# Kernel tuning notes

Measured on AMD Instinct MI355X. Metric: run time of the kernel, lower is better.

Reference implementation:

```python
import jax, jax.numpy as jnp
import numpy as np

B, H_IN, W_IN = 8192, 26, 26

def _conv(x, w, b):
    # NCHW conv, stride 1, padding 1 (as in OffConv2d: padding hardcoded to 1)
    y = jax.lax.conv_general_dilated(x, w, (1, 1), [(1, 1), (1, 1)],
                                     dimension_numbers=('NCHW', 'OIHW', 'NCHW'))
    return y + b[None, :, None, None]

def _grid_sample_bilinear_zeros(img, gx, gy):
    # img: (N,H,W), gx/gy: (N,H,W) normalized coords; matches torch grid_sample
    # mode='bilinear', padding_mode='zeros', align_corners=False
    N, H, W = img.shape
    ix = ((gx + 1.0) * W - 1.0) * 0.5
    iy = ((gy + 1.0) * H - 1.0) * 0.5
    x0 = jnp.floor(ix); y0 = jnp.floor(iy)
    x1 = x0 + 1.0;      y1 = y0 + 1.0
    wx1 = ix - x0; wx0 = 1.0 - wx1
    wy1 = iy - y0; wy0 = 1.0 - wy1
    bi = jnp.arange(N)[:, None, None]
    def gather(yy, xx):
        valid = (xx >= 0) & (xx < W) & (yy >= 0) & (yy < H)
        v = img[bi,
                jnp.clip(yy, 0, H - 1).astype(jnp.int32),
                jnp.clip(xx, 0, W - 1).astype(jnp.int32)]
        return jnp.where(valid, v, 0.0)
    return (gather(y0, x0) * wy0 * wx0 + gather(y0, x1) * wy0 * wx1 +
            gather(y1, x0) * wy1 * wx0 + gather(y1, x1) * wy1 * wx1)

def _off_conv(x, ws, bs, wx, bx, wy, by):
    s  = _conv(x, ws, bs)   # score  (B,C,H,W)
    gx = _conv(x, wx, bx)   # offset_x -> grid x coord
    gy = _conv(x, wy, by)   # offset_y -> grid y coord
    b, c, h, w = s.shape
    out = _grid_sample_bilinear_zeros(s.reshape(b * c, h, w),
                                      gx.reshape(b * c, h, w),
                                      gy.reshape(b * c, h, w))
    return out.reshape(b, c, h, w)

def _maxpool2(x):
    return jax.lax.reduce_window(x, -jnp.inf, jax.lax.max,
                                 (1, 1, 2, 2), (1, 1, 2, 2), 'VALID')

def setup_inputs() -> dict:
    key = jax.random.key(0)
    ks = jax.random.split(key, 20)
    r = lambda k, shp, s: (jax.random.normal(k, shp, dtype=jnp.float32) * s)
    inp = {
        'x':   r(ks[0], (B, H_IN, W_IN), 1.0),
        'w1s': r(ks[1], (6, 1, 5, 5), 0.2),  'b1s': r(ks[2], (6,), 0.1),
        'w1x': r(ks[3], (6, 1, 5, 5), 0.2),  'b1x': r(ks[4], (6,), 0.1),
        'w1y': r(ks[5], (6, 1, 5, 5), 0.2),  'b1y': r(ks[6], (6,), 0.1),
        'w2s': r(ks[7], (16, 6, 5, 5), 0.1), 'b2s': r(ks[8], (16,), 0.1),
        'w2x': r(ks[9], (16, 6, 5, 5), 0.1), 'b2x': r(ks[10], (16,), 0.1),
        'w2y': r(ks[11], (16, 6, 5, 5), 0.1),'b2y': r(ks[12], (16,), 0.1),
        'wf1': r(ks[13], (120, 400), 0.05),  'bf1': r(ks[14], (120,), 0.05),
        'wf2': r(ks[15], (84, 120), 0.05),   'bf2': r(ks[16], (84,), 0.05),
        'wf3': r(ks[17], (10, 84), 0.05),    'bf3': r(ks[18], (10,), 0.05),
    }
    return inp

def reference(x, w1s, b1s, w1x, b1x, w1y, b1y,
              w2s, b2s, w2x, b2x, w2y, b2y,
              wf1, bf1, wf2, bf2, wf3, bf3):
    h = x[:, None, :, :]                                   # (B,1,26,26)
    h = _maxpool2(jax.nn.relu(_off_conv(h, w1s, b1s, w1x, b1x, w1y, b1y)))  # (B,6,12,12)
    h = _maxpool2(jax.nn.relu(_off_conv(h, w2s, b2s, w2x, b2x, w2y, b2y)))  # (B,16,5,5)
    h = h.reshape(-1, 16 * 5 * 5)
    h = jax.nn.relu(h @ wf1.T + bf1)
    h = jax.nn.relu(h @ wf2.T + bf2)
    h = h @ wf3.T + bf3
    return jax.nn.softmax(h, axis=1)
```

## Files before the change

### kernel.cpp

```cpp
#include <hip/hip_runtime.h>
#include <math.h>

#define TPB 256
#define TPBA 448
#define TPBC 512

#define XS_S   34
#define SM1_S  26
#define SM1_C  624
#define H1P_R  18
#define H1P_C  252
#define H1P_I  1512

typedef float v2f __attribute__((ext_vector_type(2)));

__device__ __forceinline__ void pk_lo(v2f& acc, v2f ap, v2f w) {
    asm("v_pk_fma_f32 %0, %1, %2, %0 op_sel:[0,0,0] op_sel_hi:[0,1,1]"
        : "+v"(acc) : "v"(ap), "v"(w));
}
__device__ __forceinline__ void pk_hi(v2f& acc, v2f ap, v2f w) {
    asm("v_pk_fma_f32 %0, %1, %2, %0 op_sel:[1,0,0] op_sel_hi:[1,1,1]"
        : "+v"(acc) : "v"(ap), "v"(w));
}

#define OFF_WA_SX 0
#define OFF_WA_YY 300
#define OFF_WB_SX 464
#define OFF_WB_YY 5264
#define OFF_WF1T  7664
#define OFF_WF2T  55664
#define OFF_WF3T  65744
#define OFF_H1    66592
#define OFF_H2    7144480
#define WS_FLOATS 10421280ull
#define REQ_WS_BYTES (WS_FLOATS * 4ull)

__device__ __forceinline__ float bilin_zero_s(const float* __restrict__ img, int N, int S,
                                              float gx, float gy) {
    float fx = (gx + 1.0f) * (0.5f * (float)N) - 0.5f;
    float fy = (gy + 1.0f) * (0.5f * (float)N) - 0.5f;
    float x0 = floorf(fx), y0 = floorf(fy);
    float wx1 = fx - x0, wy1 = fy - y0;
    float wx0 = 1.0f - wx1, wy0 = 1.0f - wy1;
    float x1 = x0 + 1.0f, y1 = y0 + 1.0f;
    float Nm1 = (float)(N - 1);
    int xi0 = (int)fminf(fmaxf(x0, 0.0f), Nm1);
    int yi0 = (int)fminf(fmaxf(y0, 0.0f), Nm1);
    int xi1 = (int)fminf(fmaxf(x1, 0.0f), Nm1);
    int yi1 = (int)fminf(fmaxf(y1, 0.0f), Nm1);
    bool vx0 = (x0 >= 0.0f) && (x0 < (float)N);
    bool vx1 = (x1 >= 0.0f) && (x1 < (float)N);
    bool vy0 = (y0 >= 0.0f) && (y0 < (float)N);
    bool vy1 = (y1 >= 0.0f) && (y1 < (float)N);
    float v00 = (vy0 && vx0) ? img[yi0 * S + xi0] : 0.0f;
    float v01 = (vy0 && vx1) ? img[yi0 * S + xi1] : 0.0f;
    float v10 = (vy1 && vx0) ? img[yi1 * S + xi0] : 0.0f;
    float v11 = (vy1 && vx1) ? img[yi1 * S + xi1] : 0.0f;
    return v00 * wy0 * wx0 + v01 * wy0 * wx1 + v10 * wy1 * wx0 + v11 * wy1 * wx1;
}

__global__ __launch_bounds__(TPB) void lenet_prep(
    const float* __restrict__ w1s, const float* __restrict__ w1x, const float* __restrict__ w1y,
    const float* __restrict__ w2s, const float* __restrict__ w2x, const float* __restrict__ w2y,
    const float* __restrict__ wf1, const float* __restrict__ wf2, const float* __restrict__ wf3,
    float* __restrict__ wsf)
{
    int g = blockIdx.x * TPB + threadIdx.x;
    int stride = gridDim.x * TPB;
    for (int i = g; i < 75; i += stride) {
        int cp = i / 25, t = i % 25;
        int cA = (2 * cp) * 25 + t, cB = (2 * cp + 1) * 25 + t;
        float* p = wsf + OFF_WA_SX + i * 4;
        p[0] = w1s[cA]; p[1] = w1x[cA]; p[2] = w1s[cB]; p[3] = w1x[cB];
        wsf[OFF_WA_YY + i * 2 + 0] = w1y[cA];
        wsf[OFF_WA_YY + i * 2 + 1] = w1y[cB];
    }
    for (int e = g; e < 1200; e += stride) {
        int cp = e / 150, rem = e % 150;
        int iA = cp * 150 + rem, iB = (cp + 8) * 150 + rem;
        float* pp = wsf + OFF_WB_SX + e * 4;
        pp[0] = w2s[iA]; pp[1] = w2s[iB]; pp[2] = w2x[iA]; pp[3] = w2x[iB];
        wsf[OFF_WB_YY + e * 2 + 0] = w2y[iA];
        wsf[OFF_WB_YY + e * 2 + 1] = w2y[iB];
    }
    for (int i = g; i < 48000; i += stride) { int k = i / 120, o = i % 120; wsf[OFF_WF1T + i] = wf1[o * 400 + k]; }
    for (int i = g; i < 10080; i += stride) { int k = i / 84,  o = i % 84;  wsf[OFF_WF2T + i] = wf2[o * 120 + k]; }
    for (int i = g; i < 840;   i += stride) { int k = i / 10,  o = i % 10;  wsf[OFF_WF3T + i] = wf3[o * 84 + k]; }
}

__global__ __launch_bounds__(TPBA) void lenetA(
    const float* __restrict__ x, const float* __restrict__ wsf,
    const float* __restrict__ b1s, const float* __restrict__ b1x, const float* __restrict__ b1y,
    float* __restrict__ h1)
{
    __shared__ __align__(16) float xs_p[28 * XS_S];
    __shared__ float4 w1i[150];
    __shared__ float4 b1w[3];
    __shared__ v2f    b1yw[3];
    __shared__ __align__(16) float smap1[6 * SM1_C];

    const int tid = threadIdx.x, b = blockIdx.x;
    const float* xp = x + b * 676;
    for (int i = tid; i < 28 * XS_S; i += TPBA) {
        int r = i / XS_S, c = i % XS_S;
        float v = 0.0f;
        if (c < 28 && r >= 1 && r <= 26 && c >= 1 && c <= 26) v = xp[(r - 1) * 26 + (c - 1)];
        xs_p[i] = v;
    }
    if (tid < 150) w1i[tid] = ((const float4*)(wsf + OFF_WA_SX))[tid];
    if (tid < 3) {
        b1w[tid]  = make_float4(b1s[2 * tid], b1x[2 * tid], b1s[2 * tid + 1], b1x[2 * tid + 1]);
        b1yw[tid] = (v2f){b1y[2 * tid], b1y[2 * tid + 1]};
    }
    __syncthreads();

    const v2f* wyy = (const v2f*)(wsf + OFF_WA_YY);

    const int cp = tid / 144, p = tid % 144;
    const int py = p / 12, px = p % 12;
    const bool act = (tid < 432);

    float gxa[2][2][2], gya[2][2][2];
    if (act) {
        v2f aw[6][3];
        #pragma unroll
        for (int r = 0; r < 6; ++r) {
            const v2f* rp = (const v2f*)&xs_p[(2 * py + r) * XS_S + 2 * px];
            aw[r][0] = rp[0]; aw[r][1] = rp[1]; aw[r][2] = rp[2];
        }
        int c0 = 2 * cp, c1 = 2 * cp + 1;
        v2f a0[2][2], a1[2][2], ay[2][2];
        {
            float4 bb = b1w[cp];
            v2f i0 = {bb.x, bb.y};
            v2f i1 = {bb.z, bb.w};
            v2f iy = b1yw[cp];
            #pragma unroll
            for (int dy = 0; dy < 2; ++dy)
                #pragma unroll
                for (int dx = 0; dx < 2; ++dx) { a0[dy][dx] = i0; a1[dy][dx] = i1; ay[dy][dx] = iy; }
        }
        const float4* wp  = &w1i[cp * 25];
        const v2f*    wyp = wyy + cp * 25;
        #pragma unroll
        for (int ky = 0; ky < 5; ++ky)
            #pragma unroll
            for (int kx = 0; kx < 5; ++kx) {
                float4 w4 = wp[ky * 5 + kx];
                v2f wA = {w4.x, w4.y};
                v2f wB = {w4.z, w4.w};
                v2f wy = wyp[ky * 5 + kx];
                #pragma unroll
                for (int dy = 0; dy < 2; ++dy)
                    #pragma unroll
                    for (int dx = 0; dx < 2; ++dx) {
                        int cc = kx + dx;
                        v2f ap = aw[ky + dy][cc >> 1];
                        if ((cc & 1) == 0) {
                            pk_lo(a0[dy][dx], ap, wA);
                            pk_lo(a1[dy][dx], ap, wB);
                            pk_lo(ay[dy][dx], ap, wy);
                        } else {
                            pk_hi(a0[dy][dx], ap, wA);
                            pk_hi(a1[dy][dx], ap, wB);
                            pk_hi(ay[dy][dx], ap, wy);
                        }
                    }
            }
        {
            int base0 = (2 * py) * SM1_S + 2 * px;
            int base1 = base0 + SM1_S;
            *(v2f*)&smap1[c0 * SM1_C + base0] = (v2f){a0[0][0].x, a0[0][1].x};
            *(v2f*)&smap1[c0 * SM1_C + base1] = (v2f){a0[1][0].x, a0[1][1].x};
            *(v2f*)&smap1[c1 * SM1_C + base0] = (v2f){a1[0][0].x, a1[0][1].x};
            *(v2f*)&smap1[c1 * SM1_C + base1] = (v2f){a1[1][0].x, a1[1][1].x};
        }
        #pragma unroll
        for (int dy = 0; dy < 2; ++dy)
            #pragma unroll
            for (int dx = 0; dx < 2; ++dx) {
                gxa[0][dy][dx] = a0[dy][dx].y;  gya[0][dy][dx] = ay[dy][dx].x;
                gxa[1][dy][dx] = a1[dy][dx].y;  gya[1][dy][dx] = ay[dy][dx].y;
            }
    }
    __syncthreads();

    if (act) {
        #pragma unroll
        for (int ch = 0; ch < 2; ++ch) {
            int c = 2 * cp + ch;
            const float* smc = &smap1[c * SM1_C];
            float mx = 0.0f;
            #pragma unroll
            for (int dy = 0; dy < 2; ++dy)
                #pragma unroll
                for (int dx = 0; dx < 2; ++dx)
                    mx = fmaxf(mx, bilin_zero_s(smc, 24, SM1_S, gxa[ch][dy][dx], gya[ch][dy][dx]));
            h1[(size_t)b * 864 + c * 144 + p] = mx;
        }
    }
}

__global__ __launch_bounds__(TPB, 6) void lenetB(
    const float* __restrict__ h1, const float* __restrict__ wsf,
    const float* __restrict__ b2s, const float* __restrict__ b2x, const float* __restrict__ b2y,
    float* __restrict__ h2)
{
    __shared__ __align__(16) float h1p[2 * H1P_I];
    __shared__ __align__(16) float wsm[4][2][2][100];

    const int tid = threadIdx.x, b = blockIdx.x;

    for (int i = tid; i < 2 * H1P_I; i += TPB) {
        int im = i / H1P_I;
        int k = i - im * H1P_I;
        int ch = k / H1P_C, p2 = k % H1P_C;
        int r = p2 / H1P_R, c = p2 % H1P_R;
        float v = 0.0f;
        if (c < 14 && r >= 1 && r <= 12 && c >= 1 && c <= 12)
            v = h1[(size_t)(2 * b + im) * 864 + ch * 144 + (r - 1) * 12 + (c - 1)];
        h1p[i] = v;
    }
    __syncthreads();

    const int lane = tid & 63;
    const int wvu  = __builtin_amdgcn_readfirstlane(tid >> 6);
    const int img  = lane >> 5;
    const int p    = lane & 31;
    const bool act = (p < 25);
    const int py = p / 5, px = p % 5;

    const float4* wsx = (const float4*)(wsf + OFF_WB_SX);
    const v2f*    wyy = (const v2f*)   (wsf + OFF_WB_YY);
    float* smw = &wsm[wvu][img][0][0];
    const float* h1pi = &h1p[img * H1P_I];

    #pragma unroll
    for (int rep = 0; rep < 2; ++rep) {
        const int cp = wvu + 4 * rep;
        if (rep) {
            asm volatile("s_waitcnt lgkmcnt(0)" ::: "memory");
            __builtin_amdgcn_sched_barrier(0);
        }
        float s0[2][2], s1[2][2], x0[2][2], x1[2][2], y0[2][2], y1[2][2];
        if (act) {
            {
                float is0 = b2s[cp], is1 = b2s[cp + 8];
                float ix0 = b2x[cp], ix1 = b2x[cp + 8];
                float iy0 = b2y[cp], iy1 = b2y[cp + 8];
                #pragma unroll
                for (int dy = 0; dy < 2; ++dy)
                    #pragma unroll
                    for (int dx = 0; dx < 2; ++dx) {
                        s0[dy][dx] = is0; s1[dy][dx] = is1;
                        x0[dy][dx] = ix0; x1[dy][dx] = ix1;
                        y0[dy][dx] = iy0; y1[dy][dx] = iy1;
                    }
            }
            #pragma unroll
            for (int i = 0; i < 6; ++i) {
                v2f aw[6][3];
                #pragma unroll
                for (int r = 0; r < 6; ++r) {
                    const v2f* rp = (const v2f*)&h1pi[i * H1P_C + (2 * py + r) * H1P_R + 2 * px];
                    aw[r][0] = rp[0]; aw[r][1] = rp[1]; aw[r][2] = rp[2];
                }
                const float4* wt  = wsx + (cp * 6 + i) * 25;
                const v2f*    wyt = wyy + (cp * 6 + i) * 25;
                #pragma unroll
                for (int ky = 0; ky < 5; ++ky)
                    #pragma unroll
                    for (int kx = 0; kx < 5; ++kx) {
                        float4 w4 = wt[ky * 5 + kx];
                        v2f    wy = wyt[ky * 5 + kx];
                        #pragma unroll
                        for (int dy = 0; dy < 2; ++dy)
                            #pragma unroll
                            for (int dx = 0; dx < 2; ++dx) {
                                int cc = kx + dx;
                                v2f ap = aw[ky + dy][cc >> 1];
                                float av = (cc & 1) ? ap.y : ap.x;
                                s0[dy][dx] = fmaf(av, w4.x, s0[dy][dx]);
                                s1[dy][dx] = fmaf(av, w4.y, s1[dy][dx]);
                                x0[dy][dx] = fmaf(av, w4.z, x0[dy][dx]);
                                x1[dy][dx] = fmaf(av, w4.w, x1[dy][dx]);
                                y0[dy][dx] = fmaf(av, wy.x, y0[dy][dx]);
                                y1[dy][dx] = fmaf(av, wy.y, y1[dy][dx]);
                            }
                    }
            }
            {
                int base0 = (2 * py) * 10 + 2 * px;
                int base1 = base0 + 10;
                *(v2f*)&smw[base0]       = (v2f){s0[0][0], s0[0][1]};
                *(v2f*)&smw[base1]       = (v2f){s0[1][0], s0[1][1]};
                *(v2f*)&smw[100 + base0] = (v2f){s1[0][0], s1[0][1]};
                *(v2f*)&smw[100 + base1] = (v2f){s1[1][0], s1[1][1]};
            }
        }
        asm volatile("s_waitcnt lgkmcnt(0)" ::: "memory");
        __builtin_amdgcn_sched_barrier(0);
        if (act) {
            #pragma unroll
            for (int slot = 0; slot < 2; ++slot) {
                int c = cp + slot * 8;
                const float* smc = &smw[slot * 100];
                float mx = 0.0f;
                #pragma unroll
                for (int dy = 0; dy < 2; ++dy)
                    #pragma unroll
                    for (int dx = 0; dx < 2; ++dx) {
                        float gx = slot ? x1[dy][dx] : x0[dy][dx];
                        float gy = slot ? y1[dy][dx] : y0[dy][dx];
                        mx = fmaxf(mx, bilin_zero_s(smc, 10, 10, gx, gy));
                    }
                h2[(size_t)(2 * b + img) * 400 + c * 25 + p] = mx;
            }
        }
    }
}

__global__ __launch_bounds__(TPBC) void lenetC(
    const float* __restrict__ h2, const float* __restrict__ wsf,
    const float* __restrict__ bf1, const float* __restrict__ bf2, const float* __restrict__ bf3,
    float* __restrict__ out)
{
    __shared__ __align__(16) float h2s[8][2][400];
    __shared__ float f1s[8][2][120];
    __shared__ float f2s[8][2][84];
    __shared__ float f3s[8][2][10];

    const int tid = threadIdx.x;
    const int w = tid >> 6, lane = tid & 63;
    const int img0 = blockIdx.x * 16 + w * 2;

    for (int j = 0; j < 2; ++j) {
        float4*       dst = (float4*)&h2s[w][j][0];
        const float4* src = (const float4*)&h2[(img0 + j) * 400];
        for (int k = lane; k < 100; k += 64) dst[k] = src[k];
    }
    __syncthreads();

    {
        const float* wf1T = wsf + OFF_WF1T;
        float acc1[2] = {0, 0}, acc2[2] = {0, 0};
        for (int k = 0; k < 400; ++k) {
            float wa = wf1T[k * 120 + lane];
            float wb = (lane < 56) ? wf1T[k * 120 + 64 + lane] : 0.0f;
            #pragma unroll
            for (int j = 0; j < 2; ++j) {
                float hv = h2s[w][j][k];
                acc1[j] = fmaf(hv, wa, acc1[j]);
                acc2[j] = fmaf(hv, wb, acc2[j]);
            }
        }
        float bb1 = bf1[lane];
        float bb2 = (lane < 56) ? bf1[64 + lane] : 0.0f;
        #pragma unroll
        for (int j = 0; j < 2; ++j) {
            f1s[w][j][lane] = fmaxf(acc1[j] + bb1, 0.0f);
            if (lane < 56) f1s[w][j][64 + lane] = fmaxf(acc2[j] + bb2, 0.0f);
        }
    }
    __syncthreads();

    {
        const float* wf2T = wsf + OFF_WF2T;
        float acc1[2], acc2[2];
        float bb1 = bf2[lane];
        float bb2 = (lane < 20) ? bf2[64 + lane] : 0.0f;
        #pragma unroll
        for (int j = 0; j < 2; ++j) { acc1[j] = bb1; acc2[j] = bb2; }
        for (int k = 0; k < 120; ++k) {
            float wa = wf2T[k * 84 + lane];
            float wb = (lane < 20) ? wf2T[k * 84 + 64 + lane] : 0.0f;
            #pragma unroll
            for (int j = 0; j < 2; ++j) {
                float hv = f1s[w][j][k];
                acc1[j] = fmaf(hv, wa, acc1[j]);
                acc2[j] = fmaf(hv, wb, acc2[j]);
            }
        }
        #pragma unroll
        for (int j = 0; j < 2; ++j) {
            f2s[w][j][lane] = fmaxf(acc1[j], 0.0f);
            if (lane < 20) f2s[w][j][64 + lane] = fmaxf(acc2[j], 0.0f);
        }
    }
    __syncthreads();

    if (lane < 10) {
        const float* wf3T = wsf + OFF_WF3T;
        float acc[2];
        float bb = bf3[lane];
        #pragma unroll
        for (int j = 0; j < 2; ++j) acc[j] = bb;
        for (int k = 0; k < 84; ++k) {
            float wv = wf3T[k * 10 + lane];
            #pragma unroll
            for (int j = 0; j < 2; ++j) acc[j] = fmaf(f2s[w][j][k], wv, acc[j]);
        }
        #pragma unroll
        for (int j = 0; j < 2; ++j) f3s[w][j][lane] = acc[j];
    }
    __syncthreads();

    if (lane < 20) {
        int j = lane / 10, c = lane % 10;
        float m = f3s[w][j][0];
        #pragma unroll
        for (int q = 1; q < 10; ++q) m = fmaxf(m, f3s[w][j][q]);
        float ssum = 0.0f;
        #pragma unroll
        for (int q = 0; q < 10; ++q) ssum += expf(f3s[w][j][q] - m);
        out[(img0 + j) * 10 + c] = expf(f3s[w][j][c] - m) / ssum;
    }
}

__global__ __launch_bounds__(TPB, 2) void lenet_off_fused(
    const float* __restrict__ x,
    const float* __restrict__ w1s, const float* __restrict__ b1s,
    const float* __restrict__ w1x, const float* __restrict__ b1x,
    const float* __restrict__ w1y, const float* __restrict__ b1y,
    const float* __restrict__ w2s, const float* __restrict__ b2s,
    const float* __restrict__ w2x, const float* __restrict__ b2x,
    const float* __restrict__ w2y, const float* __restrict__ b2y,
    const float* __restrict__ wf1, const float* __restrict__ bf1,
    const float* __restrict__ wf2, const float* __restrict__ bf2,
    const float* __restrict__ wf3, const float* __restrict__ bf3,
    float* __restrict__ out)
{
    __shared__ __align__(16) float  xs_p[784];
    __shared__ float4 w1i[150];
    __shared__ float4 b1i[6];
    __shared__ float4 w2i[2400];
    __shared__ float4 b2i[16];
    __shared__ __align__(16) float  smap1[3456];
    __shared__ __align__(16) float  h1p[1176];
    __shared__ __align__(16) float  smap2[1600];
    __shared__ __align__(16) float  h2[400];
    __shared__ __align__(16) float  f1[120];
    __shared__ __align__(16) float  f2[84];
    __shared__ float  f3[10];

    const int tid = threadIdx.x;
    const int b   = blockIdx.x;

    const float* xp = x + b * 676;
    for (int i = tid; i < 784; i += TPB) {
        int r = i / 28, c = i % 28;
        float v = 0.0f;
        if (r >= 1 && r <= 26 && c >= 1 && c <= 26) v = xp[(r - 1) * 26 + (c - 1)];
        xs_p[i] = v;
    }
    for (int i = tid; i < 150; i += TPB)
        w1i[i] = make_float4(w1s[i], w1x[i], w1y[i], 0.0f);
    if (tid < 6)  b1i[tid] = make_float4(b1s[tid], b1x[tid], b1y[tid], 0.0f);
    for (int i = tid; i < 2400; i += TPB)
        w2i[i] = make_float4(w2s[i], w2x[i], w2y[i], 0.0f);
    if (tid < 16) b2i[tid] = make_float4(b2s[tid], b2x[tid], b2y[tid], 0.0f);
    for (int i = tid; i < 1176; i += TPB) h1p[i] = 0.0f;
    __syncthreads();

    float gxr[4][2][2], gyr[4][2][2];
    #pragma unroll
    for (int it = 0; it < 4; ++it) {
        int idx = tid + it * TPB;
        if (idx < 864) {
            int c = idx / 144, p = idx % 144;
            int py = p / 12, px = p % 12;
            float a[6][6];
            #pragma unroll
            for (int r = 0; r < 6; ++r) {
                const float2* rp = (const float2*)&xs_p[(2 * py + r) * 28 + 2 * px];
                float2 v0 = rp[0], v1 = rp[1], v2 = rp[2];
                a[r][0] = v0.x; a[r][1] = v0.y; a[r][2] = v1.x;
                a[r][3] = v1.y; a[r][4] = v2.x; a[r][5] = v2.y;
            }
            float4 bb = b1i[c];
            float s[2][2], agx[2][2], agy[2][2];
            #pragma unroll
            for (int dy = 0; dy < 2; ++dy)
                #pragma unroll
                for (int dx = 0; dx < 2; ++dx) { s[dy][dx] = bb.x; agx[dy][dx] = bb.y; agy[dy][dx] = bb.z; }
            #pragma unroll
            for (int ky = 0; ky < 5; ++ky)
                #pragma unroll
                for (int kx = 0; kx < 5; ++kx) {
                    float4 w = w1i[c * 25 + ky * 5 + kx];
                    #pragma unroll
                    for (int dy = 0; dy < 2; ++dy)
                        #pragma unroll
                        for (int dx = 0; dx < 2; ++dx) {
                            float v = a[ky + dy][kx + dx];
                            s[dy][dx]   = fmaf(v, w.x, s[dy][dx]);
                            agx[dy][dx] = fmaf(v, w.y, agx[dy][dx]);
                            agy[dy][dx] = fmaf(v, w.z, agy[dy][dx]);
                        }
                }
            float* sm = &smap1[c * 576 + (2 * py) * 24 + 2 * px];
            sm[0] = s[0][0]; sm[1] = s[0][1]; sm[24] = s[1][0]; sm[25] = s[1][1];
            #pragma unroll
            for (int dy = 0; dy < 2; ++dy)
                #pragma unroll
                for (int dx = 0; dx < 2; ++dx) { gxr[it][dy][dx] = agx[dy][dx]; gyr[it][dy][dx] = agy[dy][dx]; }
        }
    }
    __syncthreads();

    #pragma unroll
    for (int it = 0; it < 4; ++it) {
        int idx = tid + it * TPB;
        if (idx < 864) {
            int c = idx / 144, p = idx % 144;
            int py = p / 12, px = p % 12;
            const float* smc = &smap1[c * 576];
            float mx = 0.0f;
            #pragma unroll
            for (int dy = 0; dy < 2; ++dy)
                #pragma unroll
                for (int dx = 0; dx < 2; ++dx)
                    mx = fmaxf(mx, bilin_zero_s(smc, 24, 24, gxr[it][dy][dx], gyr[it][dy][dx]));
            h1p[c * 196 + (py + 1) * 14 + (px + 1)] = mx;
        }
    }
    __syncthreads();

    float gxr2[2][2][2], gyr2[2][2][2];
    #pragma unroll
    for (int it = 0; it < 2; ++it) {
        int idx = tid + it * TPB;
        if (idx < 400) {
            int c = idx / 25, p = idx % 25;
            int py = p / 5, px = p % 5;
            float4 bb = b2i[c];
            float s[2][2], agx[2][2], agy[2][2];
            #pragma unroll
            for (int dy = 0; dy < 2; ++dy)
                #pragma unroll
                for (int dx = 0; dx < 2; ++dx) { s[dy][dx] = bb.x; agx[dy][dx] = bb.y; agy[dy][dx] = bb.z; }
            for (int i = 0; i < 6; ++i) {
                float a[6][6];
                #pragma unroll
                for (int r = 0; r < 6; ++r) {
                    const float2* rp = (const float2*)&h1p[i * 196 + (2 * py + r) * 14 + 2 * px];
                    float2 v0 = rp[0], v1 = rp[1], v2 = rp[2];
                    a[r][0] = v0.x; a[r][1] = v0.y; a[r][2] = v1.x;
                    a[r][3] = v1.y; a[r][4] = v2.x; a[r][5] = v2.y;
                }
                const float4* wc = &w2i[c * 150 + i * 25];
                #pragma unroll
                for (int ky = 0; ky < 5; ++ky)
                    #pragma unroll
                    for (int kx = 0; kx < 5; ++kx) {
                        float4 w = wc[ky * 5 + kx];
                        #pragma unroll
                        for (int dy = 0; dy < 2; ++dy)
                            #pragma unroll
                            for (int dx = 0; dx < 2; ++dx) {
                                float v = a[ky + dy][kx + dx];
                                s[dy][dx]   = fmaf(v, w.x, s[dy][dx]);
                                agx[dy][dx] = fmaf(v, w.y, agx[dy][dx]);
                                agy[dy][dx] = fmaf(v, w.z, agy[dy][dx]);
                            }
                    }
            }
            float* sm = &smap2[c * 100 + (2 * py) * 10 + 2 * px];
            sm[0] = s[0][0]; sm[1] = s[0][1]; sm[10] = s[1][0]; sm[11] = s[1][1];
            #pragma unroll
            for (int dy = 0; dy < 2; ++dy)
                #pragma unroll
                for (int dx = 0; dx < 2; ++dx) { gxr2[it][dy][dx] = agx[dy][dx]; gyr2[it][dy][dx] = agy[dy][dx]; }
        }
    }
    __syncthreads();

    #pragma unroll
    for (int it = 0; it < 2; ++it) {
        int idx = tid + it * TPB;
        if (idx < 400) {
            int c = idx / 25, p = idx % 25;
            int py = p / 5, px = p % 5;
            const float* smc = &smap2[c * 100];
            float mx = 0.0f;
            #pragma unroll
            for (int dy = 0; dy < 2; ++dy)
                #pragma unroll
                for (int dx = 0; dx < 2; ++dx)
                    mx = fmaxf(mx, bilin_zero_s(smc, 10, 10, gxr2[it][dy][dx], gyr2[it][dy][dx]));
            h2[c * 25 + py * 5 + px] = mx;
        }
    }
    __syncthreads();

    if (tid < 240) {
        int o = tid >> 1, h = tid & 1;
        const float4* wrow = (const float4*)(wf1 + o * 400 + h * 200);
        const float4* hh   = (const float4*)&h2[h * 200];
        float acc = 0.0f;
        for (int k = 0; k < 50; ++k) {
            float4 w = wrow[k]; float4 v = hh[k];
            acc = fmaf(w.x, v.x, acc); acc = fmaf(w.y, v.y, acc);
            acc = fmaf(w.z, v.z, acc); acc = fmaf(w.w, v.w, acc);
        }
        acc += __shfl_xor(acc, 1);
        if (h == 0) f1[o] = fmaxf(acc + bf1[o], 0.0f);
    }
    __syncthreads();

    if (tid < 84) {
        const float4* wrow = (const float4*)(wf2 + tid * 120);
        const float4* hh   = (const float4*)f1;
        float acc = bf2[tid];
        for (int k = 0; k < 30; ++k) {
            float4 w = wrow[k]; float4 v = hh[k];
            acc = fmaf(w.x, v.x, acc); acc = fmaf(w.y, v.y, acc);
            acc = fmaf(w.z, v.z, acc); acc = fmaf(w.w, v.w, acc);
        }
        f2[tid] = fmaxf(acc, 0.0f);
    }
    __syncthreads();

    if (tid < 10) {
        const float4* wrow = (const float4*)(wf3 + tid * 84);
        const float4* hh   = (const float4*)f2;
        float acc = bf3[tid];
        for (int k = 0; k < 21; ++k) {
            float4 w = wrow[k]; float4 v = hh[k];
            acc = fmaf(w.x, v.x, acc); acc = fmaf(w.y, v.y, acc);
            acc = fmaf(w.z, v.z, acc); acc = fmaf(w.w, v.w, acc);
        }
        f3[tid] = acc;
    }
    __syncthreads();

    if (tid < 10) {
        float m = f3[0];
        #pragma unroll
        for (int j = 1; j < 10; ++j) m = fmaxf(m, f3[j]);
        float ssum = 0.0f;
        #pragma unroll
        for (int j = 0; j < 10; ++j) ssum += expf(f3[j] - m);
        out[b * 10 + tid] = expf(f3[tid] - m) / ssum;
    }
}

extern "C" void kernel_launch(void* const* d_in, const int* in_sizes, int n_in,
                              void* d_out, int out_size, void* d_ws, size_t ws_size,
                              hipStream_t stream) {
    const float* x   = (const float*)d_in[0];
    const float* w1s = (const float*)d_in[1];
    const float* b1s = (const float*)d_in[2];
    const float* w1x = (const float*)d_in[3];
    const float* b1x = (const float*)d_in[4];
    const float* w1y = (const float*)d_in[5];
    const float* b1y = (const float*)d_in[6];
    const float* w2s = (const float*)d_in[7];
    const float* b2s = (const float*)d_in[8];
    const float* w2x = (const float*)d_in[9];
    const float* b2x = (const float*)d_in[10];
    const float* w2y = (const float*)d_in[11];
    const float* b2y = (const float*)d_in[12];
    const float* wf1 = (const float*)d_in[13];
    const float* bf1 = (const float*)d_in[14];
    const float* wf2 = (const float*)d_in[15];
    const float* bf2 = (const float*)d_in[16];
    const float* wf3 = (const float*)d_in[17];
    const float* bf3 = (const float*)d_in[18];
    float* out = (float*)d_out;

    if (ws_size >= REQ_WS_BYTES) {
        float* wsf = (float*)d_ws;
        lenet_prep<<<64, TPB, 0, stream>>>(w1s, w1x, w1y, w2s, w2x, w2y,
                                           wf1, wf2, wf3, wsf);
        lenetA<<<8192, TPBA, 0, stream>>>(x, wsf, b1s, b1x, b1y, wsf + OFF_H1);
        lenetB<<<4096, TPB, 0, stream>>>(wsf + OFF_H1, wsf, b2s, b2x, b2y, wsf + OFF_H2);
        lenetC<<<512, TPBC, 0, stream>>>(wsf + OFF_H2, wsf, bf1, bf2, bf3, out);
    } else {
        lenet_off_fused<<<8192, TPB, 0, stream>>>(
            x, w1s, b1s, w1x, b1x, w1y, b1y,
            w2s, b2s, w2x, b2x, w2y, b2y,
            wf1, bf1, wf2, bf2, wf3, bf3, out);
    }
}
```

Baseline: 309.0 us.

## Compute four conv2 channels per pass in lenetB with rolling row buffer

Merges the two channel-pair passes of lenetB into one pass where each thread accumulates score, x and y for four output channels at once. Each input row is loaded from LDS once and reused across all four channels, using a two-row rolling buffer instead of holding all six rows in registers. This halves LDS activation reads and removes one sync point per block. The cost is a doubled accumulator set (48 floats), so occupancy is lowered from 6 to 4 waves per SIMD and the shared scratch buffer doubles in size.

New measurement: 626.3 us. +102.7%, slower.

```diff
diff --git a/kernel.cpp b/kernel.cpp
--- a/kernel.cpp
+++ b/kernel.cpp
@@ -201,13 +201,13 @@
     }
 }
 
-__global__ __launch_bounds__(TPB, 6) void lenetB(
+__global__ __launch_bounds__(TPB, 4) void lenetB(
     const float* __restrict__ h1, const float* __restrict__ wsf,
     const float* __restrict__ b2s, const float* __restrict__ b2x, const float* __restrict__ b2y,
     float* __restrict__ h2)
 {
     __shared__ __align__(16) float h1p[2 * H1P_I];
-    __shared__ __align__(16) float wsm[4][2][2][100];
+    __shared__ __align__(16) float wsm[4][2][4][100];
 
     const int tid = threadIdx.x, b = blockIdx.x;
 
@@ -235,87 +235,91 @@
     float* smw = &wsm[wvu][img][0][0];
     const float* h1pi = &h1p[img * H1P_I];
 
-    #pragma unroll
-    for (int rep = 0; rep < 2; ++rep) {
-        const int cp = wvu + 4 * rep;
-        if (rep) {
-            asm volatile("s_waitcnt lgkmcnt(0)" ::: "memory");
-            __builtin_amdgcn_sched_barrier(0);
-        }
-        float s0[2][2], s1[2][2], x0[2][2], x1[2][2], y0[2][2], y1[2][2];
-        if (act) {
-            {
-                float is0 = b2s[cp], is1 = b2s[cp + 8];
-                float ix0 = b2x[cp], ix1 = b2x[cp + 8];
-                float iy0 = b2y[cp], iy1 = b2y[cp + 8];
-                #pragma unroll
-                for (int dy = 0; dy < 2; ++dy)
+    float sa[4][2][2], ga[4][2][2], ya[4][2][2];
+    if (act) {
+        #pragma unroll
+        for (int j = 0; j < 4; ++j) {
+            int c = wvu + 4 * j;
+            float is = b2s[c], ix = b2x[c], iy = b2y[c];
+            #pragma unroll
+            for (int dy = 0; dy < 2; ++dy)
+                #pragma unroll
+                for (int dx = 0; dx < 2; ++dx) { sa[j][dy][dx] = is; ga[j][dy][dx] = ix; ya[j][dy][dx] = iy; }
+        }
+        #pragma unroll
+        for (int i = 0; i < 6; ++i) {
+            const float4* wtA = wsx + (((wvu)     * 6) + i) * 25;
+            const float4* wtB = wsx + (((wvu + 4) * 6) + i) * 25;
+            const v2f*    wyA = wyy + (((wvu)     * 6) + i) * 25;
+            const v2f*    wyB = wyy + (((wvu + 4) * 6) + i) * 25;
+            const float*  base = &h1pi[i * H1P_C + (2 * py) * H1P_R + 2 * px];
+
+            v2f rA[3], rB[3];
+            auto loadrow = [&](v2f* d, int r) {
+                const v2f* rp = (const v2f*)&base[r * H1P_R];
+                d[0] = rp[0]; d[1] = rp[1]; d[2] = rp[2];
+            };
+            auto dorow = [&](const v2f* rlo, const v2f* rhi, int ky) {
+                #pragma unroll
+                for (int kx = 0; kx < 5; ++kx) {
+                    float4 wa = wtA[ky * 5 + kx];
+                    float4 wb = wtB[ky * 5 + kx];
+                    v2f    va = wyA[ky * 5 + kx];
+                    v2f    vb = wyB[ky * 5 + kx];
                     #pragma unroll
-                    for (int dx = 0; dx < 2; ++dx) {
-                        s0[dy][dx] = is0; s1[dy][dx] = is1;
-                        x0[dy][dx] = ix0; x1[dy][dx] = ix1;
-                        y0[dy][dx] = iy0; y1[dy][dx] = iy1;
+                    for (int dy = 0; dy < 2; ++dy) {
+                        const v2f* row = dy ? rhi : rlo;
+                        #pragma unroll
+                        for (int dx = 0; dx < 2; ++dx) {
+                            int cc = kx + dx;
+                            v2f ap = row[cc >> 1];
+                            float av = (cc & 1) ? ap.y : ap.x;
+                            sa[0][dy][dx] = fmaf(av, wa.x, sa[0][dy][dx]);
+                            sa[2][dy][dx] = fmaf(av, wa.y, sa[2][dy][dx]);
+                            ga[0][dy][dx] = fmaf(av, wa.z, ga[0][dy][dx]);
+                            ga[2][dy][dx] = fmaf(av, wa.w, ga[2][dy][dx]);
+                            sa[1][dy][dx] = fmaf(av, wb.x, sa[1][dy][dx]);
+                            sa[3][dy][dx] = fmaf(av, wb.y, sa[3][dy][dx]);
+                            ga[1][dy][dx] = fmaf(av, wb.z, ga[1][dy][dx]);
+                            ga[3][dy][dx] = fmaf(av, wb.w, ga[3][dy][dx]);
+                            ya[0][dy][dx] = fmaf(av, va.x, ya[0][dy][dx]);
+                            ya[2][dy][dx] = fmaf(av, va.y, ya[2][dy][dx]);
+                            ya[1][dy][dx] = fmaf(av, vb.x, ya[1][dy][dx]);
+                            ya[3][dy][dx] = fmaf(av, vb.y, ya[3][dy][dx]);
+                        }
                     }
+                }
+            };
+            loadrow(rA, 0); loadrow(rB, 1); dorow(rA, rB, 0);
+            loadrow(rA, 2);                 dorow(rB, rA, 1);
+            loadrow(rB, 3);                 dorow(rA, rB, 2);
+            loadrow(rA, 4);                 dorow(rB, rA, 3);
+            loadrow(rB, 5);                 dorow(rA, rB, 4);
+        }
+        {
+            int base0 = (2 * py) * 10 + 2 * px;
+            int base1 = base0 + 10;
+            #pragma unroll
+            for (int j = 0; j < 4; ++j) {
+                *(v2f*)&smw[j * 100 + base0] = (v2f){sa[j][0][0], sa[j][0][1]};
+                *(v2f*)&smw[j * 100 + base1] = (v2f){sa[j][1][0], sa[j][1][1]};
             }
-            #pragma unroll
-            for (int i = 0; i < 6; ++i) {
-                v2f aw[6][3];
-                #pragma unroll
-                for (int r = 0; r < 6; ++r) {
-                    const v2f* rp = (const v2f*)&h1pi[i * H1P_C + (2 * py + r) * H1P_R + 2 * px];
-                    aw[r][0] = rp[0]; aw[r][1] = rp[1]; aw[r][2] = rp[2];
-                }
-                const float4* wt  = wsx + (cp * 6 + i) * 25;
-                const v2f*    wyt = wyy + (cp * 6 + i) * 25;
-                #pragma unroll
-                for (int ky = 0; ky < 5; ++ky)
-                    #pragma unroll
-                    for (int kx = 0; kx < 5; ++kx) {
-                        float4 w4 = wt[ky * 5 + kx];
-                        v2f    wy = wyt[ky * 5 + kx];
-                        #pragma unroll
-                        for (int dy = 0; dy < 2; ++dy)
-                            #pragma unroll
-                            for (int dx = 0; dx < 2; ++dx) {
-                                int cc = kx + dx;
-                                v2f ap = aw[ky + dy][cc >> 1];
-                                float av = (cc & 1) ? ap.y : ap.x;
-                                s0[dy][dx] = fmaf(av, w4.x, s0[dy][dx]);
-                                s1[dy][dx] = fmaf(av, w4.y, s1[dy][dx]);
-                                x0[dy][dx] = fmaf(av, w4.z, x0[dy][dx]);
-                                x1[dy][dx] = fmaf(av, w4.w, x1[dy][dx]);
-                                y0[dy][dx] = fmaf(av, wy.x, y0[dy][dx]);
-                                y1[dy][dx] = fmaf(av, wy.y, y1[dy][dx]);
-                            }
-                    }
-            }
-            {
-                int base0 = (2 * py) * 10 + 2 * px;
-                int base1 = base0 + 10;
-                *(v2f*)&smw[base0]       = (v2f){s0[0][0], s0[0][1]};
-                *(v2f*)&smw[base1]       = (v2f){s0[1][0], s0[1][1]};
-                *(v2f*)&smw[100 + base0] = (v2f){s1[0][0], s1[0][1]};
-                *(v2f*)&smw[100 + base1] = (v2f){s1[1][0], s1[1][1]};
-            }
-        }
-        asm volatile("s_waitcnt lgkmcnt(0)" ::: "memory");
-        __builtin_amdgcn_sched_barrier(0);
-        if (act) {
-            #pragma unroll
-            for (int slot = 0; slot < 2; ++slot) {
-                int c = cp + slot * 8;
-                const float* smc = &smw[slot * 100];
-                float mx = 0.0f;
-                #pragma unroll
-                for (int dy = 0; dy < 2; ++dy)
-                    #pragma unroll
-                    for (int dx = 0; dx < 2; ++dx) {
-                        float gx = slot ? x1[dy][dx] : x0[dy][dx];
-                        float gy = slot ? y1[dy][dx] : y0[dy][dx];
-                        mx = fmaxf(mx, bilin_zero_s(smc, 10, 10, gx, gy));
-                    }
-                h2[(size_t)(2 * b + img) * 400 + c * 25 + p] = mx;
-            }
+        }
+    }
+    asm volatile("s_waitcnt lgkmcnt(0)" ::: "memory");
+    __builtin_amdgcn_sched_barrier(0);
+    if (act) {
+        #pragma unroll
+        for (int j = 0; j < 4; ++j) {
+            int c = wvu + 4 * j;
+            const float* smc = &smw[j * 100];
+            float mx = 0.0f;
+            #pragma unroll
+            for (int dy = 0; dy < 2; ++dy)
+                #pragma unroll
+                for (int dx = 0; dx < 2; ++dx)
+                    mx = fmaxf(mx, bilin_zero_s(smc, 10, 10, ga[j][dy][dx], ya[j][dy][dx]));
+            h2[(size_t)(2 * b + img) * 400 + c * 25 + p] = mx;
         }
     }
 }
```
